# Kernel tuning notes

Hardware: AMD Instinct MI355X
Metric: run time of the kernel (lower is better)

The kernel has to match this reference:

```python
import jax, jax.numpy as jnp
import numpy as np
from functools import partial

# Straight-through-estimator binarization: forward hard threshold,
# backward identity (matches BinaPs BinarizeTensorThresh autograd.Function).
@partial(jax.custom_vjp, nondiff_argnums=(1,))
def binarize(x, thresh):
    return (x >= thresh).astype(x.dtype)

def _bin_fwd(x, thresh):
    return binarize(x, thresh), None

def _bin_bwd(thresh, res, g):
    return (g,)

binarize.defvjp(_bin_fwd, _bin_bwd)

WEIGHT_THRESH = 0.5   # weightBClipValue passed to BinarizedLinearModule
ACT_THRESH = 1.0      # binary activation fires when pre-activation reaches 1


def setup_inputs() -> dict:
    key = jax.random.key(0)
    kx, kw = jax.random.split(key)
    B, D, H = 8192, 4096, 2048  # batch (transactions), features, hidden (patterns)
    x = (jax.random.uniform(kx, (B, D)) < 0.05).astype(jnp.float32)
    # Real-valued shared encoder weight, clipped to [-1, 1] by clipWeights();
    # init in [0, 1) so its 0.5-threshold binarization is non-trivial.
    W = jax.random.uniform(kw, (H, D), dtype=jnp.float32)
    b_enc = -jnp.ones((H,), jnp.float32)   # init_bias: vector of -1
    b0 = jnp.zeros((H,), jnp.float32)      # act0 bias (clipBias keeps <= 0)
    b3 = jnp.zeros((D,), jnp.float32)      # act3 bias (noBias forces 0)
    return {"x": x, "W": W, "b_enc": b_enc, "b0": b0, "b3": b3}


def reference(x, W, b_enc, b0, b3):
    # Binarize shared weight (encoder and transposed decoder use the same Wb)
    Wb = binarize(W, WEIGHT_THRESH)                      # [H, D] in {0,1}
    # Encoder: BinarizedLinear(D->H) with bias, then BinaryActivation
    h = binarize(x @ Wb.T + b_enc + b0, ACT_THRESH)      # [B, H] in {0,1}
    # Decoder: transposed shared weight, no bias, then final BinaryActivation
    out = binarize(h @ Wb + b3, ACT_THRESH)              # [B, D] in {0,1}
    return out
```

## Files before the change

kernel.cpp:

```cpp
#include <hip/hip_runtime.h>
#include <stdint.h>

#define BB 8192
#define DD 4096
#define HH 2048
#define DW (DD / 32)
#define HW (HH / 32)

__global__ void k_pack_x(const float* __restrict__ x,
                         uint32_t* __restrict__ xb) {
    int flat = blockIdx.x * blockDim.x + threadIdx.x;
    int b  = flat >> 7;
    int wd = flat & (DW - 1);
    const float4* p = (const float4*)(x + (size_t)b * DD + 32 * wd);
    uint32_t w = 0;
#pragma unroll
    for (int q = 0; q < 8; ++q) {
        float4 v = p[q];
        w |= (v.x >= 0.5f ? 1u : 0u) << (4 * q + 0);
        w |= (v.y >= 0.5f ? 1u : 0u) << (4 * q + 1);
        w |= (v.z >= 0.5f ? 1u : 0u) << (4 * q + 2);
        w |= (v.w >= 0.5f ? 1u : 0u) << (4 * q + 3);
    }
    xb[flat] = w;
}

__global__ void k_pack_wrow(const float* __restrict__ W,
                            uint32_t* __restrict__ WrowT4) {
    int flat = blockIdx.x * blockDim.x + threadIdx.x;
    int j = flat >> 7;
    int k = flat & (DW - 1);
    const float4* p = (const float4*)(W + (size_t)j * DD + 32 * k);
    uint32_t w = 0;
#pragma unroll
    for (int q = 0; q < 8; ++q) {
        float4 v = p[q];
        w |= (v.x >= 0.5f ? 1u : 0u) << (4 * q + 0);
        w |= (v.y >= 0.5f ? 1u : 0u) << (4 * q + 1);
        w |= (v.z >= 0.5f ? 1u : 0u) << (4 * q + 2);
        w |= (v.w >= 0.5f ? 1u : 0u) << (4 * q + 3);
    }
    WrowT4[((size_t)(k >> 2) * HH + j) * 4 + (k & 3)] = w;
}

__global__ void k_pack_wcol(const float* __restrict__ W,
                            uint32_t* __restrict__ WcolT) {
    int flat = blockIdx.x * blockDim.x + threadIdx.x;
    int kw = flat >> 12;
    int d  = flat & (DD - 1);
    uint32_t w = 0;
#pragma unroll
    for (int i = 0; i < 32; ++i) {
        float v = W[(size_t)(kw * 32 + i) * DD + d];
        w |= (v >= 0.5f ? 1u : 0u) << i;
    }
    WcolT[(size_t)kw * DD + d] = w;
}

__device__ __forceinline__ int calc_thresh(float bias) {
    float need = 1.0f - bias;
    if (!(need == need)) return 2000000000;
    if (need > 1.0e9f)  return 2000000000;
    if (need < -1.0e9f) return -2000000000;
    int t = (int)ceilf(need);
#pragma unroll
    for (int it = 0; it < 2; ++it)
        if ((float)(t - 1) + bias >= 1.0f) t--;
#pragma unroll
    for (int it = 0; it < 2; ++it)
        if ((float)t + bias < 1.0f) t++;
    return t;
}

__global__ void k_thresh(const float* __restrict__ b_enc,
                         const float* __restrict__ b0,
                         const float* __restrict__ b3,
                         int* __restrict__ t1, int* __restrict__ t2) {
    int tid = blockIdx.x * blockDim.x + threadIdx.x;
    if (tid < HH) {
        t1[tid] = calc_thresh(b_enc[tid] + b0[tid]);
    } else {
        int d = tid - HH;
        t2[d] = calc_thresh(b3[d]);
    }
}

__global__ void k_gemm1(const uint32_t* __restrict__ xb,
                        const uint4* __restrict__ WrowT4,
                        const int* __restrict__ t1,
                        uint32_t* __restrict__ hb) {
    int flat = blockIdx.x * blockDim.x + threadIdx.x;
    int b = flat >> 11;
    int j = flat & (HH - 1);
    const uint32_t* xr = xb + (size_t)b * DW;
    int t = t1[j];
    int c = 0;
    if (t > 0) {
        for (int k4 = 0; k4 < DW / 4; ++k4) {
            uint4 w = WrowT4[(size_t)k4 * HH + j];
            uint4 a = *(const uint4*)(xr + 4 * k4);
            c += __popc(a.x & w.x) + __popc(a.y & w.y) +
                 __popc(a.z & w.z) + __popc(a.w & w.w);
            if (c >= t) break;
        }
    }
    unsigned long long m = __ballot(c >= t);
    if ((threadIdx.x & 63) == 0) {
        int jw = j >> 5;
        hb[(size_t)b * HW + jw]     = (uint32_t)m;
        hb[(size_t)b * HW + jw + 1] = (uint32_t)(m >> 32);
    }
}

__global__ void k_gemm2(const uint32_t* __restrict__ hb,
                        const uint32_t* __restrict__ WcolT,
                        const int* __restrict__ t2,
                        float* __restrict__ out) {
    int flat = blockIdx.x * blockDim.x + threadIdx.x;
    int b  = flat >> 10;
    int d0 = (flat & 1023) * 4;
    const uint32_t* hr = hb + (size_t)b * HW;
    int4 tt = *(const int4*)(t2 + d0);
    int c0 = 0, c1 = 0, c2 = 0, c3 = 0;
    for (int kw = 0; kw < HW; ++kw) {
        if (c0 >= tt.x && c1 >= tt.y && c2 >= tt.z && c3 >= tt.w) break;
        uint32_t hw = hr[kw];
        uint4 w = *(const uint4*)(WcolT + (size_t)kw * DD + d0);
        c0 += __popc(hw & w.x);
        c1 += __popc(hw & w.y);
        c2 += __popc(hw & w.z);
        c3 += __popc(hw & w.w);
    }
    float4 r;
    r.x = (c0 >= tt.x) ? 1.0f : 0.0f;
    r.y = (c1 >= tt.y) ? 1.0f : 0.0f;
    r.z = (c2 >= tt.z) ? 1.0f : 0.0f;
    r.w = (c3 >= tt.w) ? 1.0f : 0.0f;
    *(float4*)(out + (size_t)b * DD + d0) = r;
}

extern "C" void kernel_launch(void* const* d_in, const int* in_sizes, int n_in,
                              void* d_out, int out_size, void* d_ws, size_t ws_size,
                              hipStream_t stream) {
    const float* x     = (const float*)d_in[0];
    const float* W     = (const float*)d_in[1];
    const float* b_enc = (const float*)d_in[2];
    const float* b0    = (const float*)d_in[3];
    const float* b3    = (const float*)d_in[4];
    float* out = (float*)d_out;

    char* ws = (char*)d_ws;
    uint32_t* WrowT4 = (uint32_t*)(ws);
    uint32_t* WcolT  = (uint32_t*)(ws + (1u << 20));
    uint32_t* xb     = (uint32_t*)(ws + (2u << 20));
    uint32_t* hb     = (uint32_t*)(ws + (6u << 20));
    int*      t1     = (int*)(ws + (8u << 20));
    int*      t2     = (int*)(ws + (8u << 20) + 8192);

    const int BLK = 256;

    k_pack_wrow<<<(HH * DW) / BLK, BLK, 0, stream>>>(W, WrowT4);
    k_pack_wcol<<<(HW * DD) / BLK, BLK, 0, stream>>>(W, WcolT);
    k_pack_x  <<<(BB * DW) / BLK, BLK, 0, stream>>>(x, xb);
    k_thresh  <<<(HH + DD) / BLK, BLK, 0, stream>>>(b_enc, b0, b3, t1, t2);
    k_gemm1   <<<(BB * HH) / BLK, BLK, 0, stream>>>(xb, (const uint4*)WrowT4, t1, hb);
    k_gemm2   <<<(BB * DD / 4) / BLK, BLK, 0, stream>>>(hb, WcolT, t2, out);
}
```

Before: 324.7 us.

## Fuse x packing, both binary GEMMs into one per-row kernel with LDS

Packs x with wave ballots straight into shared memory, then runs the encoder popcount GEMM and the decoder popcount GEMM inside one block per batch row, keeping the hidden bitmask in LDS. This removes the global round trips for the packed x and h buffers and two kernel launches. In exchange, each block is one 256-thread row, so per-row work is serialized across loops, and parallelism per launch changes. Early-exit divergence within waves may also differ.

```diff
diff --git a/kernel.cpp b/kernel.cpp
--- a/kernel.cpp
+++ b/kernel.cpp
@@ -6,24 +6,6 @@
 #define HH 2048
 #define DW (DD / 32)
 #define HW (HH / 32)
-
-__global__ void k_pack_x(const float* __restrict__ x,
-                         uint32_t* __restrict__ xb) {
-    int flat = blockIdx.x * blockDim.x + threadIdx.x;
-    int b  = flat >> 7;
-    int wd = flat & (DW - 1);
-    const float4* p = (const float4*)(x + (size_t)b * DD + 32 * wd);
-    uint32_t w = 0;
-#pragma unroll
-    for (int q = 0; q < 8; ++q) {
-        float4 v = p[q];
-        w |= (v.x >= 0.5f ? 1u : 0u) << (4 * q + 0);
-        w |= (v.y >= 0.5f ? 1u : 0u) << (4 * q + 1);
-        w |= (v.z >= 0.5f ? 1u : 0u) << (4 * q + 2);
-        w |= (v.w >= 0.5f ? 1u : 0u) << (4 * q + 3);
-    }
-    xb[flat] = w;
-}
 
 __global__ void k_pack_wrow(const float* __restrict__ W,
                             uint32_t* __restrict__ WrowT4) {
@@ -85,58 +67,79 @@
     }
 }
 
-__global__ void k_gemm1(const uint32_t* __restrict__ xb,
-                        const uint4* __restrict__ WrowT4,
-                        const int* __restrict__ t1,
-                        uint32_t* __restrict__ hb) {
-    int flat = blockIdx.x * blockDim.x + threadIdx.x;
-    int b = flat >> 11;
-    int j = flat & (HH - 1);
-    const uint32_t* xr = xb + (size_t)b * DW;
-    int t = t1[j];
-    int c = 0;
-    if (t > 0) {
-        for (int k4 = 0; k4 < DW / 4; ++k4) {
-            uint4 w = WrowT4[(size_t)k4 * HH + j];
-            uint4 a = *(const uint4*)(xr + 4 * k4);
-            c += __popc(a.x & w.x) + __popc(a.y & w.y) +
-                 __popc(a.z & w.z) + __popc(a.w & w.w);
-            if (c >= t) break;
+__global__ void __launch_bounds__(256)
+k_main(const float* __restrict__ x,
+       const uint4* __restrict__ WrowT4,
+       const uint32_t* __restrict__ WcolT,
+       const int* __restrict__ t1,
+       const int* __restrict__ t2,
+       float* __restrict__ out) {
+    __shared__ uint32_t xw[DW];
+    __shared__ uint32_t hw[HW];
+
+    const int b   = blockIdx.x;
+    const int tid = threadIdx.x;
+    const int wv  = tid >> 6;
+    const int ln  = tid & 63;
+
+    const float* xr = x + (size_t)b * DD;
+#pragma unroll
+    for (int it = 0; it < 16; ++it) {
+        int d = it * 256 + tid;
+        unsigned long long m = __ballot(xr[d] >= 0.5f);
+        if (ln == 0) {
+            int wd = it * 8 + wv * 2;
+            xw[wd]     = (uint32_t)m;
+            xw[wd + 1] = (uint32_t)(m >> 32);
         }
     }
-    unsigned long long m = __ballot(c >= t);
-    if ((threadIdx.x & 63) == 0) {
-        int jw = j >> 5;
-        hb[(size_t)b * HW + jw]     = (uint32_t)m;
-        hb[(size_t)b * HW + jw + 1] = (uint32_t)(m >> 32);
+    __syncthreads();
+
+    for (int jj = 0; jj < 8; ++jj) {
+        int j = jj * 256 + tid;
+        int t = t1[j];
+        int c = 0;
+        if (t > 0) {
+            for (int k4 = 0; k4 < DW / 4; ++k4) {
+                uint4 w = WrowT4[(size_t)k4 * HH + j];
+                uint4 a = *(const uint4*)(xw + 4 * k4);
+                c += __popc(a.x & w.x) + __popc(a.y & w.y) +
+                     __popc(a.z & w.z) + __popc(a.w & w.w);
+                if (c >= t) break;
+            }
+        }
+        unsigned long long m = __ballot(c >= t);
+        if (ln == 0) {
+            int wd = jj * 8 + wv * 2;
+            hw[wd]     = (uint32_t)m;
+            hw[wd + 1] = (uint32_t)(m >> 32);
+        }
     }
-}
+    __syncthreads();
 
-__global__ void k_gemm2(const uint32_t* __restrict__ hb,
-                        const uint32_t* __restrict__ WcolT,
-                        const int* __restrict__ t2,
-                        float* __restrict__ out) {
-    int flat = blockIdx.x * blockDim.x + threadIdx.x;
-    int b  = flat >> 10;
-    int d0 = (flat & 1023) * 4;
-    const uint32_t* hr = hb + (size_t)b * HW;
-    int4 tt = *(const int4*)(t2 + d0);
-    int c0 = 0, c1 = 0, c2 = 0, c3 = 0;
-    for (int kw = 0; kw < HW; ++kw) {
-        if (c0 >= tt.x && c1 >= tt.y && c2 >= tt.z && c3 >= tt.w) break;
-        uint32_t hw = hr[kw];
-        uint4 w = *(const uint4*)(WcolT + (size_t)kw * DD + d0);
-        c0 += __popc(hw & w.x);
-        c1 += __popc(hw & w.y);
-        c2 += __popc(hw & w.z);
-        c3 += __popc(hw & w.w);
+    float* orow = out + (size_t)b * DD;
+#pragma unroll
+    for (int it = 0; it < 4; ++it) {
+        int q  = it * 256 + tid;
+        int d0 = q * 4;
+        int4 tt = *(const int4*)(t2 + d0);
+        int c0 = 0, c1 = 0, c2 = 0, c3 = 0;
+        for (int kw = 0; kw < HW; ++kw) {
+            if (c0 >= tt.x && c1 >= tt.y && c2 >= tt.z && c3 >= tt.w) break;
+            uint32_t h = hw[kw];
+            uint4 w = *(const uint4*)(WcolT + (size_t)kw * DD + d0);
+            c0 += __popc(h & w.x);
+            c1 += __popc(h & w.y);
+            c2 += __popc(h & w.z);
+            c3 += __popc(h & w.w);
+        }
+        float4 r;
+        r.x = (c0 >= tt.x) ? 1.0f : 0.0f;
+        r.y = (c1 >= tt.y) ? 1.0f : 0.0f;
+        r.z = (c2 >= tt.z) ? 1.0f : 0.0f;
+        r.w = (c3 >= tt.w) ? 1.0f : 0.0f;
+        *(float4*)(orow + d0) = r;
     }
-    float4 r;
-    r.x = (c0 >= tt.x) ? 1.0f : 0.0f;
-    r.y = (c1 >= tt.y) ? 1.0f : 0.0f;
-    r.z = (c2 >= tt.z) ? 1.0f : 0.0f;
-    r.w = (c3 >= tt.w) ? 1.0f : 0.0f;
-    *(float4*)(out + (size_t)b * DD + d0) = r;
 }
 
 extern "C" void kernel_launch(void* const* d_in, const int* in_sizes, int n_in,
@@ -152,17 +155,13 @@
     char* ws = (char*)d_ws;
     uint32_t* WrowT4 = (uint32_t*)(ws);
     uint32_t* WcolT  = (uint32_t*)(ws + (1u << 20));
-    uint32_t* xb     = (uint32_t*)(ws + (2u << 20));
-    uint32_t* hb     = (uint32_t*)(ws + (6u << 20));
-    int*      t1     = (int*)(ws + (8u << 20));
-    int*      t2     = (int*)(ws + (8u << 20) + 8192);
+    int*      t1     = (int*)(ws + (2u << 20));
+    int*      t2     = (int*)(ws + (2u << 20) + 8192);
 
     const int BLK = 256;
 
     k_pack_wrow<<<(HH * DW) / BLK, BLK, 0, stream>>>(W, WrowT4);
     k_pack_wcol<<<(HW * DD) / BLK, BLK, 0, stream>>>(W, WcolT);
-    k_pack_x  <<<(BB * DW) / BLK, BLK, 0, stream>>>(x, xb);
     k_thresh  <<<(HH + DD) / BLK, BLK, 0, stream>>>(b_enc, b0, b3, t1, t2);
-    k_gemm1   <<<(BB * HH) / BLK, BLK, 0, stream>>>(xb, (const uint4*)WrowT4, t1, hb);
-    k_gemm2   <<<(BB * DD / 4) / BLK, BLK, 0, stream>>>(hb, WcolT, t2, out);
+    k_main    <<<BB, BLK, 0, stream>>>(x, (const uint4*)WrowT4, WcolT, t1, t2, out);
 }
```

After: 432.2 us. 33.1% more time.
